# Kernel tuning notes

Hardware: AMD Instinct MI355X
Metric: run time of the kernel (lower is better)

## Reference

```python
import math
import jax, jax.numpy as jnp
import numpy as np

B, N, D, O = 8, 2048, 128, 128


def setup_inputs() -> dict:
    key = jax.random.key(0)
    ks = jax.random.split(key, 8)
    s = 1.0 / math.sqrt(D)
    x = jax.random.normal(ks[0], (B, N, D), dtype=jnp.float32)
    A = jax.random.bernoulli(ks[1], 0.02, (B, N, N)).astype(jnp.float32)
    W_qk = jax.random.normal(ks[2], (D, D), dtype=jnp.float32) * s
    b_qk = jnp.zeros((D,), dtype=jnp.float32)
    W_l = jax.random.normal(ks[3], (D, O), dtype=jnp.float32) * s
    b_l = jnp.zeros((O,), dtype=jnp.float32)
    W_r = jax.random.normal(ks[4], (D, O), dtype=jnp.float32) * s
    W_d = jax.random.normal(ks[5], (1, D), dtype=jnp.float32)
    b_d = jnp.zeros((D,), dtype=jnp.float32)
    return {"x": x, "A": A, "W_qk": W_qk, "b_qk": b_qk, "W_l": W_l,
            "b_l": b_l, "W_r": W_r, "W_d": W_d, "b_d": b_d}


def reference(x, A, W_qk, b_qk, W_l, b_l, W_r, W_d, b_d):
    d = x.shape[-1]
    # degree gate: sigmoid(Linear(deg)) scales features
    deg = jnp.sum(A, axis=-1, keepdims=True)              # (B,N,1)
    gate = jax.nn.sigmoid(deg @ W_d + b_d)                # (B,N,D)
    xg = x * gate                                         # (B,N,D)
    # sigmoid QK projection and dense NxN scores
    QK = jax.nn.sigmoid(xg @ W_qk + b_qk)                 # (B,N,D)
    scores = jnp.einsum('bnd,bmd->bnm', QK, QK) / jnp.sqrt(jnp.float32(d))
    scores = scores * A                                   # adjacency mask
    attn = scores / (jnp.sum(scores, axis=-1, keepdims=True) + 1e-6)
    agg = jnp.einsum('bnm,bmd->bnd', attn, xg)            # (B,N,D)
    out = agg @ W_l + b_l + xg @ W_r                      # (B,N,O)
    # F.normalize(p=2, dim=-1): x / max(||x||, eps)
    nrm = jnp.linalg.norm(out, axis=-1, keepdims=True)
    return out / jnp.maximum(nrm, 1e-12)
```

## Files before the change

### kernel.cpp

```cpp
#include <hip/hip_runtime.h>
#include <hip/hip_bf16.h>

#define B_ 8
#define N_ 2048
#define D_ 128
#define NROW (B_*N_)

typedef __bf16 bf16;
typedef __bf16 bf16x8 __attribute__((ext_vector_type(8)));
typedef float f32x4 __attribute__((ext_vector_type(4)));
typedef float f32x16 __attribute__((ext_vector_type(16)));

__device__ __forceinline__ float sigmoidf_(float x) {
    return 1.0f / (1.0f + __expf(-x));
}

__device__ __forceinline__ void g2l16(const bf16* g, void* l) {
    __builtin_amdgcn_global_load_lds(
        (const __attribute__((address_space(1))) unsigned int*)g,
        (__attribute__((address_space(3))) unsigned int*)l, 16, 0, 0);
}

__device__ __forceinline__ unsigned pk_bf16(float a, float b) {
    union { bf16 h[2]; unsigned u; } t;
    t.h[0] = (bf16)a; t.h[1] = (bf16)b;
    return t.u;
}

__global__ __launch_bounds__(256) void k_wtrans(const float* __restrict__ Wqk,
        const float* __restrict__ Wl, const float* __restrict__ Wr,
        bf16* __restrict__ wqkT, bf16* __restrict__ wlT, bf16* __restrict__ wrT) {
    int m = blockIdx.x >> 3;
    int chunk = blockIdx.x & 7;
    const float* W = (m == 0) ? Wqk : (m == 1 ? Wl : Wr);
    bf16* WT = (m == 0) ? wqkT : (m == 1 ? wlT : wrT);
#pragma unroll
    for (int e = 0; e < 8; ++e) {
        int idx = e * 256 + threadIdx.x;
        int ol = idx >> 7;
        int i  = idx & 127;
        int o = chunk * 16 + ol;
        WT[o * 128 + i] = (bf16)W[i * 128 + o];
    }
}

__global__ __launch_bounds__(256) void k_deg_mask(const float* __restrict__ A,
        unsigned int* __restrict__ mask, float* __restrict__ deg) {
    const int row = blockIdx.x;
    const float* a = A + (size_t)row * N_;
    const int t = threadIdx.x, w = t >> 6, lane = t & 63;
    __shared__ int partial[4];
    int cnt = 0;
    unsigned int* mrow = mask + (size_t)row * (N_ / 32);
#pragma unroll
    for (int i = 0; i < N_ / 1024; ++i) {
        float4 v = *(const float4*)(a + i * 1024 + t * 4);
        unsigned long long nib = (unsigned long long)((v.x != 0.f) | ((v.y != 0.f) << 1) |
                                                      ((v.z != 0.f) << 2) | ((v.w != 0.f) << 3));
        unsigned long long p = nib << ((t & 15) * 4);
        p |= __shfl_xor(p, 1);
        p |= __shfl_xor(p, 2);
        p |= __shfl_xor(p, 4);
        p |= __shfl_xor(p, 8);
        if ((t & 15) == 0) {
            int idx = i * 32 + (t >> 4) * 2;
            mrow[idx] = (unsigned int)p;
            mrow[idx + 1] = (unsigned int)(p >> 32);
            cnt += __popcll(p);
        }
    }
    cnt += __shfl_xor(cnt, 16);
    cnt += __shfl_xor(cnt, 32);
    if (lane == 0) partial[w] = cnt;
    __syncthreads();
    if (t == 0) deg[row] = (float)(partial[0] + partial[1] + partial[2] + partial[3]);
}

__global__ __launch_bounds__(256) void k_proj(const float* __restrict__ x,
        const float* __restrict__ deg, const float* __restrict__ Wd,
        const float* __restrict__ bd, const bf16* __restrict__ wqkT,
        const float* __restrict__ bqk,
        bf16* __restrict__ qkG, bf16* __restrict__ xgG, bf16* __restrict__ xgTG) {
    __shared__ bf16 wq[128][136];
    __shared__ bf16 xgl[64][136];
    const int t = threadIdx.x, lane = t & 63, w = t >> 6;
    const int rowbase = blockIdx.x * 64;
    {
        int r = t >> 1, h = t & 1;
        const bf16* src = wqkT + r * 128 + h * 64;
#pragma unroll
        for (int k = 0; k < 64; k += 8)
            *(bf16x8*)&wq[r][h * 64 + k] = *(const bf16x8*)(src + k);
    }
#pragma unroll
    for (int e = 0; e < 32; ++e) {
        int idx = e * 256 + t;
        int rl = idx >> 7;
        int d  = idx & 127;
        size_t fr = (size_t)rowbase + rl;
        float g = sigmoidf_(deg[fr] * Wd[d] + bd[d]);
        float v = x[fr * 128 + d] * g;
        bf16 bv = (bf16)v;
        xgl[rl][d] = bv;
        xgG[fr * 128 + d] = bv;
    }
    __syncthreads();
    const int cIdx = lane & 15, g4 = lane >> 4;
    bf16x8 ax[4];
#pragma unroll
    for (int c = 0; c < 4; ++c)
        ax[c] = *(const bf16x8*)&xgl[w * 16 + cIdx][c * 32 + g4 * 8];
#pragma unroll
    for (int dsub = 0; dsub < 8; ++dsub) {
        f32x4 acc = {0.f, 0.f, 0.f, 0.f};
#pragma unroll
        for (int c = 0; c < 4; ++c) {
            bf16x8 bw = *(const bf16x8*)&wq[dsub * 16 + cIdx][c * 32 + g4 * 8];
            acc = __builtin_amdgcn_mfma_f32_16x16x32_bf16(ax[c], bw, acc, 0, 0, 0);
        }
        int col = dsub * 16 + cIdx;
        float bb = bqk[col];
#pragma unroll
        for (int r = 0; r < 4; ++r) {
            size_t row = (size_t)rowbase + w * 16 + g4 * 4 + r;
            qkG[row * 128 + col] = (bf16)sigmoidf_(acc[r] + bb);
        }
    }
    {
        int b = rowbase / N_;
        int nbase = rowbase % N_;
#pragma unroll
        for (int e = 0; e < 32; ++e) {
            int idx = e * 256 + t;
            int d  = idx >> 6;
            int nl = idx & 63;
            xgTG[((size_t)b * 128 + d) * N_ + nbase + nl] = xgl[nl][d];
        }
    }
}

__global__ __launch_bounds__(512, 2) void k_attn(const bf16* __restrict__ qkG,
        const bf16* __restrict__ xgTG, const unsigned int* __restrict__ mask32,
        bf16* __restrict__ aggG) {
    __shared__ __align__(16) char LDSC[132096];
    const int t = threadIdx.x, l = t & 63, w = t >> 6;
    const int h = l >> 5, l31 = l & 31;
    const int q = w >> 1, s = w & 1;
    const int bid = (blockIdx.x & 7) * 32 + (blockIdx.x >> 3);
    const int b = bid >> 5;
    const int rowbase = (bid & 31) * 64;
    const int R0 = rowbase + s * 32;
    const float inv = 0.08838834764831845f;

    auto do_stage = [&](int jb, int bbuf) {
        char* qdst = LDSC + bbuf * 32768 + w * 4096;
        char* xdst = LDSC + 65536 + bbuf * 32768 + w * 4096;
#pragma unroll
        for (int i = 0; i < 4; ++i) {
            int G = w * 256 + i * 64 + l;
            int j = G >> 4, g = G & 15;
            const bf16* src = qkG + ((size_t)(b * N_ + jb + j)) * 128 + ((g ^ (j & 7)) << 3);
            g2l16(src, qdst + i * 1024);
            const bf16* src2 = xgTG + ((size_t)b * 128 + j) * N_ + jb + ((g ^ (j & 7)) << 3);
            g2l16(src2, xdst + i * 1024);
        }
    };

    bf16x8 qki[8];
    {
        const bf16* srcB = qkG + ((size_t)(b * N_ + R0 + l31)) * 128 + h * 8;
#pragma unroll
        for (int sl = 0; sl < 8; ++sl) qki[sl] = *(const bf16x8*)(srcB + sl * 16);
    }
    const unsigned int* mrow = mask32 + ((size_t)(b * N_ + R0 + l31)) * (N_ / 32) + q;
    unsigned int mw = mrow[0];

    do_stage(0, 0);
    __syncthreads();

    f32x16 num[4]; num[0] = f32x16{}; num[1] = f32x16{}; num[2] = f32x16{}; num[3] = f32x16{};
    float rs = 0.f;

    for (int ts = 0; ts < 16; ++ts) {
        const int bb = ts & 1;
        unsigned int mw_n = 0;
        if (ts < 15) {
            mw_n = mrow[(ts + 1) * 4];
            do_stage((ts + 1) * 128, bb ^ 1);
        }
        const char* qb = LDSC + bb * 32768;
        const char* xb = LDSC + 65536 + bb * 32768;
        f32x16 st{};
        const int rowb = (q * 32 + l31) * 256;
#pragma unroll
        for (int sl = 0; sl < 8; ++sl) {
            bf16x8 aj = *(const bf16x8*)(qb + rowb + ((((sl << 1) | h) ^ (l & 7)) << 4));
            st = __builtin_amdgcn_mfma_f32_32x32x16_bf16(aj, qki[sl], st, 0, 0, 0);
        }
        unsigned int mws = mw >> (h * 4);
        unsigned int wpk[8];
#pragma unroll
        for (int r2 = 0; r2 < 8; ++r2) {
            const int r = r2 * 2;
            const int bit0 = (r & 3) + 8 * (r >> 2);
            float p0 = ((mws >> bit0) & 1u) ? st[r] * inv : 0.f;
            float p1 = ((mws >> (bit0 + 1)) & 1u) ? st[r + 1] * inv : 0.f;
            rs += p0 + p1;
            wpk[r2] = pk_bf16(p0, p1);
        }
        union { unsigned int u[4]; bf16x8 v; } pa0, pa1;
        pa0.u[0] = wpk[0]; pa0.u[1] = wpk[1]; pa0.u[2] = wpk[2]; pa0.u[3] = wpk[3];
        pa1.u[0] = wpk[4]; pa1.u[1] = wpk[5]; pa1.u[2] = wpk[6]; pa1.u[3] = wpk[7];
        const int xr = l & 7;
#pragma unroll
        for (int c = 0; c < 4; ++c) {
            const char* rowp = xb + (c * 32 + l31) * 256;
            union { unsigned long long d2[2]; bf16x8 v; } b0, b1;
            b0.d2[0] = *(const unsigned long long*)(rowp + (((q * 4 + 0) ^ xr) << 4) + (h << 3));
            b0.d2[1] = *(const unsigned long long*)(rowp + (((q * 4 + 1) ^ xr) << 4) + (h << 3));
            b1.d2[0] = *(const unsigned long long*)(rowp + (((q * 4 + 2) ^ xr) << 4) + (h << 3));
            b1.d2[1] = *(const unsigned long long*)(rowp + (((q * 4 + 3) ^ xr) << 4) + (h << 3));
            num[c] = __builtin_amdgcn_mfma_f32_32x32x16_bf16(pa0.v, b0.v, num[c], 0, 0, 0);
            num[c] = __builtin_amdgcn_mfma_f32_32x32x16_bf16(pa1.v, b1.v, num[c], 0, 0, 0);
        }
        mw = mw_n;
        __syncthreads();
    }

    rs += __shfl_xor(rs, 32);
    float* RSB = (float*)(LDSC + 131072);
    if (l < 32) RSB[(s * 32 + l31) * 4 + q] = rs;
    float* PART = (float*)LDSC;
#pragma unroll
    for (int c = 0; c < 4; ++c)
#pragma unroll
        for (int r = 0; r < 16; ++r) {
            int m = (r & 3) + 8 * (r >> 2) + 4 * h;
            PART[q * 8192 + (s * 32 + m) * 128 + c * 32 + l31] = num[c][r];
        }
    __syncthreads();
    {
        int row = t >> 3, colbase = (t & 7) * 16;
        float accv[16];
#pragma unroll
        for (int k = 0; k < 16; ++k) accv[k] = 0.f;
#pragma unroll
        for (int q4 = 0; q4 < 4; ++q4)
#pragma unroll
            for (int k = 0; k < 4; ++k) {
                f32x4 pv = *(const f32x4*)(PART + q4 * 8192 + row * 128 + colbase + k * 4);
                accv[k * 4 + 0] += pv[0]; accv[k * 4 + 1] += pv[1];
                accv[k * 4 + 2] += pv[2]; accv[k * 4 + 3] += pv[3];
            }
        float den = RSB[row * 4 + 0] + RSB[row * 4 + 1] + RSB[row * 4 + 2] + RSB[row * 4 + 3] + 1e-6f;
        float sc = 1.0f / den;
        bf16x8 o0, o1;
#pragma unroll
        for (int k = 0; k < 8; ++k) { o0[k] = (bf16)(accv[k] * sc); o1[k] = (bf16)(accv[8 + k] * sc); }
        bf16* dst = aggG + ((size_t)(b * N_ + rowbase + row)) * 128 + colbase;
        *(bf16x8*)dst = o0;
        *(bf16x8*)(dst + 8) = o1;
    }
}

__global__ __launch_bounds__(256) void k_out(const bf16* __restrict__ aggG,
        const bf16* __restrict__ xgG, const bf16* __restrict__ wlT,
        const bf16* __restrict__ wrT, const float* __restrict__ blv,
        float* __restrict__ out) {
    __shared__ bf16 wl[128][136];
    __shared__ bf16 wr[128][136];
    __shared__ bf16 ag[64][136];
    __shared__ bf16 xgl[64][136];
    const int t = threadIdx.x, lane = t & 63, w = t >> 6;
    const int rowbase = blockIdx.x * 64;
    {
        int r = t >> 1, h = t & 1;
#pragma unroll
        for (int k = 0; k < 64; k += 8) {
            *(bf16x8*)&wl[r][h * 64 + k] = *(const bf16x8*)(wlT + r * 128 + h * 64 + k);
            *(bf16x8*)&wr[r][h * 64 + k] = *(const bf16x8*)(wrT + r * 128 + h * 64 + k);
        }
        int rl = t >> 2, q = t & 3;
        const bf16* s1 = aggG + ((size_t)(rowbase + rl)) * 128 + q * 32;
        const bf16* s2 = xgG + ((size_t)(rowbase + rl)) * 128 + q * 32;
#pragma unroll
        for (int k = 0; k < 32; k += 8) {
            *(bf16x8*)&ag[rl][q * 32 + k] = *(const bf16x8*)(s1 + k);
            *(bf16x8*)&xgl[rl][q * 32 + k] = *(const bf16x8*)(s2 + k);
        }
    }
    __syncthreads();
    const int cIdx = lane & 15, g4 = lane >> 4;
    bf16x8 aa[4], ax[4];
#pragma unroll
    for (int c = 0; c < 4; ++c) {
        aa[c] = *(const bf16x8*)&ag[w * 16 + cIdx][c * 32 + g4 * 8];
        ax[c] = *(const bf16x8*)&xgl[w * 16 + cIdx][c * 32 + g4 * 8];
    }
    f32x4 acc[8];
    float ss[4] = {0.f, 0.f, 0.f, 0.f};
#pragma unroll
    for (int osub = 0; osub < 8; ++osub) {
        float bb = blv[osub * 16 + cIdx];
        f32x4 a = {bb, bb, bb, bb};
#pragma unroll
        for (int c = 0; c < 4; ++c) {
            bf16x8 b1 = *(const bf16x8*)&wl[osub * 16 + cIdx][c * 32 + g4 * 8];
            a = __builtin_amdgcn_mfma_f32_16x16x32_bf16(aa[c], b1, a, 0, 0, 0);
            bf16x8 b2 = *(const bf16x8*)&wr[osub * 16 + cIdx][c * 32 + g4 * 8];
            a = __builtin_amdgcn_mfma_f32_16x16x32_bf16(ax[c], b2, a, 0, 0, 0);
        }
        acc[osub] = a;
#pragma unroll
        for (int r = 0; r < 4; ++r) ss[r] += a[r] * a[r];
    }
#pragma unroll
    for (int r = 0; r < 4; ++r) {
        ss[r] += __shfl_xor(ss[r], 1);
        ss[r] += __shfl_xor(ss[r], 2);
        ss[r] += __shfl_xor(ss[r], 4);
        ss[r] += __shfl_xor(ss[r], 8);
    }
    float sc[4];
#pragma unroll
    for (int r = 0; r < 4; ++r) sc[r] = 1.0f / fmaxf(sqrtf(ss[r]), 1e-12f);
#pragma unroll
    for (int osub = 0; osub < 8; ++osub)
#pragma unroll
        for (int r = 0; r < 4; ++r) {
            size_t row = (size_t)rowbase + w * 16 + g4 * 4 + r;
            out[row * 128 + osub * 16 + cIdx] = acc[osub][r] * sc[r];
        }
}

extern "C" void kernel_launch(void* const* d_in, const int* in_sizes, int n_in,
                              void* d_out, int out_size, void* d_ws, size_t ws_size,
                              hipStream_t stream) {
    const float* x   = (const float*)d_in[0];
    const float* A   = (const float*)d_in[1];
    const float* Wqk = (const float*)d_in[2];
    const float* bqk = (const float*)d_in[3];
    const float* Wl  = (const float*)d_in[4];
    const float* bl  = (const float*)d_in[5];
    const float* Wr  = (const float*)d_in[6];
    const float* Wd  = (const float*)d_in[7];
    const float* bd  = (const float*)d_in[8];
    float* out = (float*)d_out;
    char* ws = (char*)d_ws;

    unsigned int* maskG = (unsigned int*)ws;
    float* degG = (float*)(ws + (4 << 20));
    bf16* wqkT  = (bf16*)(ws + (5 << 20));
    bf16* wlT   = (bf16*)(ws + (5 << 20) + 32768);
    bf16* wrT   = (bf16*)(ws + (5 << 20) + 65536);
    bf16* qkG   = (bf16*)(ws + (6 << 20));
    bf16* xgG   = (bf16*)(ws + (10 << 20));
    bf16* xgTG  = (bf16*)(ws + (14 << 20));
    bf16* aggG  = (bf16*)(ws + (18 << 20));

    hipLaunchKernelGGL(k_wtrans, dim3(24), dim3(256), 0, stream, Wqk, Wl, Wr, wqkT, wlT, wrT);
    hipLaunchKernelGGL(k_deg_mask, dim3(NROW), dim3(256), 0, stream, A, maskG, degG);
    hipLaunchKernelGGL(k_proj, dim3(NROW / 64), dim3(256), 0, stream,
                       x, degG, Wd, bd, wqkT, bqk, qkG, xgG, xgTG);
    hipLaunchKernelGGL(k_attn, dim3(NROW / 64), dim3(512), 0, stream, qkG, xgTG, maskG, aggG);
    hipLaunchKernelGGL(k_out, dim3(NROW / 64), dim3(256), 0, stream, aggG, xgG, wlT, wrT, bl, out);
}
```

Baseline: 255.2 us.

## Fuse output projection into attention kernel and make degree/mask one row per wave

The output projection and L2 normalization are folded into the attention kernel: the normalized aggregate is kept in LDS instead of being written to global memory and reloaded by a separate kernel. The eight waves split the 64x128 output tile by row and column halves and combine their partial squared norms through LDS. Separately, the degree/mask kernel now handles one adjacency row per wave, which removes the shared-memory reduction and the block barrier. This saves a kernel launch and the aggregate's global round trip, but enlarges LDS usage in the attention kernel, which may reduce occupancy.

```diff
diff --git a/kernel.cpp b/kernel.cpp
--- a/kernel.cpp
+++ b/kernel.cpp
@@ -46,24 +46,23 @@
 
 __global__ __launch_bounds__(256) void k_deg_mask(const float* __restrict__ A,
         unsigned int* __restrict__ mask, float* __restrict__ deg) {
-    const int row = blockIdx.x;
+    const int w = threadIdx.x >> 6, lane = threadIdx.x & 63;
+    const int row = blockIdx.x * 4 + w;
     const float* a = A + (size_t)row * N_;
-    const int t = threadIdx.x, w = t >> 6, lane = t & 63;
-    __shared__ int partial[4];
+    unsigned int* mrow = mask + (size_t)row * (N_ / 32);
     int cnt = 0;
-    unsigned int* mrow = mask + (size_t)row * (N_ / 32);
-#pragma unroll
-    for (int i = 0; i < N_ / 1024; ++i) {
-        float4 v = *(const float4*)(a + i * 1024 + t * 4);
+#pragma unroll
+    for (int i = 0; i < N_ / 256; ++i) {
+        float4 v = *(const float4*)(a + i * 256 + lane * 4);
         unsigned long long nib = (unsigned long long)((v.x != 0.f) | ((v.y != 0.f) << 1) |
                                                       ((v.z != 0.f) << 2) | ((v.w != 0.f) << 3));
-        unsigned long long p = nib << ((t & 15) * 4);
+        unsigned long long p = nib << ((lane & 15) * 4);
         p |= __shfl_xor(p, 1);
         p |= __shfl_xor(p, 2);
         p |= __shfl_xor(p, 4);
         p |= __shfl_xor(p, 8);
-        if ((t & 15) == 0) {
-            int idx = i * 32 + (t >> 4) * 2;
+        if ((lane & 15) == 0) {
+            int idx = i * 8 + (lane >> 4) * 2;
             mrow[idx] = (unsigned int)p;
             mrow[idx + 1] = (unsigned int)(p >> 32);
             cnt += __popcll(p);
@@ -71,9 +70,7 @@
     }
     cnt += __shfl_xor(cnt, 16);
     cnt += __shfl_xor(cnt, 32);
-    if (lane == 0) partial[w] = cnt;
-    __syncthreads();
-    if (t == 0) deg[row] = (float)(partial[0] + partial[1] + partial[2] + partial[3]);
+    if (lane == 0) deg[row] = (float)cnt;
 }
 
 __global__ __launch_bounds__(256) void k_proj(const float* __restrict__ x,
@@ -139,10 +136,12 @@
     }
 }
 
-__global__ __launch_bounds__(512, 2) void k_attn(const bf16* __restrict__ qkG,
+__global__ __launch_bounds__(512, 2) void k_attn_out(const bf16* __restrict__ qkG,
         const bf16* __restrict__ xgTG, const unsigned int* __restrict__ mask32,
-        bf16* __restrict__ aggG) {
-    __shared__ __align__(16) char LDSC[132096];
+        const bf16* __restrict__ xgG, const bf16* __restrict__ wlT,
+        const bf16* __restrict__ wrT, const float* __restrict__ blv,
+        float* __restrict__ out) {
+    __shared__ __align__(16) char LDSC[149504];
     const int t = threadIdx.x, l = t & 63, w = t >> 6;
     const int h = l >> 5, l31 = l & 31;
     const int q = w >> 1, s = w & 1;
@@ -257,80 +256,85 @@
         bf16x8 o0, o1;
 #pragma unroll
         for (int k = 0; k < 8; ++k) { o0[k] = (bf16)(accv[k] * sc); o1[k] = (bf16)(accv[8 + k] * sc); }
-        bf16* dst = aggG + ((size_t)(b * N_ + rowbase + row)) * 128 + colbase;
-        *(bf16x8*)dst = o0;
-        *(bf16x8*)(dst + 8) = o1;
-    }
-}
-
-__global__ __launch_bounds__(256) void k_out(const bf16* __restrict__ aggG,
-        const bf16* __restrict__ xgG, const bf16* __restrict__ wlT,
-        const bf16* __restrict__ wrT, const float* __restrict__ blv,
-        float* __restrict__ out) {
-    __shared__ bf16 wl[128][136];
-    __shared__ bf16 wr[128][136];
-    __shared__ bf16 ag[64][136];
-    __shared__ bf16 xgl[64][136];
-    const int t = threadIdx.x, lane = t & 63, w = t >> 6;
-    const int rowbase = blockIdx.x * 64;
-    {
-        int r = t >> 1, h = t & 1;
-#pragma unroll
-        for (int k = 0; k < 64; k += 8) {
-            *(bf16x8*)&wl[r][h * 64 + k] = *(const bf16x8*)(wlT + r * 128 + h * 64 + k);
-            *(bf16x8*)&wr[r][h * 64 + k] = *(const bf16x8*)(wrT + r * 128 + h * 64 + k);
-        }
-        int rl = t >> 2, q = t & 3;
-        const bf16* s1 = aggG + ((size_t)(rowbase + rl)) * 128 + q * 32;
-        const bf16* s2 = xgG + ((size_t)(rowbase + rl)) * 128 + q * 32;
+        char* AGL = LDSC + 132096;
+        *(bf16x8*)(AGL + row * 272 + colbase * 2) = o0;
+        *(bf16x8*)(AGL + row * 272 + colbase * 2 + 16) = o1;
+    }
+    __syncthreads();
+    {
+        bf16* wlds = (bf16*)LDSC;
+        bf16* wrds = (bf16*)(LDSC + 34816);
+        bf16* xgl  = (bf16*)(LDSC + 69632);
+        int r = t >> 2, hq = t & 3;
+        const bf16* s1 = wlT + r * 128 + hq * 32;
+        const bf16* s2 = wrT + r * 128 + hq * 32;
 #pragma unroll
         for (int k = 0; k < 32; k += 8) {
-            *(bf16x8*)&ag[rl][q * 32 + k] = *(const bf16x8*)(s1 + k);
-            *(bf16x8*)&xgl[rl][q * 32 + k] = *(const bf16x8*)(s2 + k);
-        }
-    }
-    __syncthreads();
-    const int cIdx = lane & 15, g4 = lane >> 4;
-    bf16x8 aa[4], ax[4];
-#pragma unroll
-    for (int c = 0; c < 4; ++c) {
-        aa[c] = *(const bf16x8*)&ag[w * 16 + cIdx][c * 32 + g4 * 8];
-        ax[c] = *(const bf16x8*)&xgl[w * 16 + cIdx][c * 32 + g4 * 8];
-    }
-    f32x4 acc[8];
-    float ss[4] = {0.f, 0.f, 0.f, 0.f};
-#pragma unroll
-    for (int osub = 0; osub < 8; ++osub) {
-        float bb = blv[osub * 16 + cIdx];
-        f32x4 a = {bb, bb, bb, bb};
+            *(bf16x8*)&wlds[r * 136 + hq * 32 + k] = *(const bf16x8*)(s1 + k);
+            *(bf16x8*)&wrds[r * 136 + hq * 32 + k] = *(const bf16x8*)(s2 + k);
+        }
+        int rl = t >> 3, cb = (t & 7) * 16;
+        const bf16* s3 = xgG + ((size_t)(b * N_ + rowbase + rl)) * 128 + cb;
+        *(bf16x8*)&xgl[rl * 136 + cb] = *(const bf16x8*)s3;
+        *(bf16x8*)&xgl[rl * 136 + cb + 8] = *(const bf16x8*)(s3 + 8);
+    }
+    __syncthreads();
+    {
+        const bf16* wlds = (const bf16*)LDSC;
+        const bf16* wrds = (const bf16*)(LDSC + 34816);
+        const bf16* xgl  = (const bf16*)(LDSC + 69632);
+        const bf16* AGLb = (const bf16*)(LDSC + 132096);
+        float* SSB = (float*)(LDSC + 87040);
+        const int cIdx = l & 15, g4 = l >> 4;
+        const int rt = (w & 3) * 16;
+        const int oh = w >> 2;
+        bf16x8 aa[4], ax[4];
 #pragma unroll
         for (int c = 0; c < 4; ++c) {
-            bf16x8 b1 = *(const bf16x8*)&wl[osub * 16 + cIdx][c * 32 + g4 * 8];
-            a = __builtin_amdgcn_mfma_f32_16x16x32_bf16(aa[c], b1, a, 0, 0, 0);
-            bf16x8 b2 = *(const bf16x8*)&wr[osub * 16 + cIdx][c * 32 + g4 * 8];
-            a = __builtin_amdgcn_mfma_f32_16x16x32_bf16(ax[c], b2, a, 0, 0, 0);
-        }
-        acc[osub] = a;
-#pragma unroll
-        for (int r = 0; r < 4; ++r) ss[r] += a[r] * a[r];
-    }
-#pragma unroll
-    for (int r = 0; r < 4; ++r) {
-        ss[r] += __shfl_xor(ss[r], 1);
-        ss[r] += __shfl_xor(ss[r], 2);
-        ss[r] += __shfl_xor(ss[r], 4);
-        ss[r] += __shfl_xor(ss[r], 8);
-    }
-    float sc[4];
-#pragma unroll
-    for (int r = 0; r < 4; ++r) sc[r] = 1.0f / fmaxf(sqrtf(ss[r]), 1e-12f);
-#pragma unroll
-    for (int osub = 0; osub < 8; ++osub)
+            aa[c] = *(const bf16x8*)(AGLb + (rt + cIdx) * 136 + c * 32 + g4 * 8);
+            ax[c] = *(const bf16x8*)(xgl + (rt + cIdx) * 136 + c * 32 + g4 * 8);
+        }
+        f32x4 acc[4];
+        float ss[4] = {0.f, 0.f, 0.f, 0.f};
+#pragma unroll
+        for (int os = 0; os < 4; ++os) {
+            int col = (oh * 4 + os) * 16 + cIdx;
+            float bb = blv[col];
+            f32x4 a = {bb, bb, bb, bb};
+#pragma unroll
+            for (int c = 0; c < 4; ++c) {
+                bf16x8 b1 = *(const bf16x8*)(wlds + col * 136 + c * 32 + g4 * 8);
+                a = __builtin_amdgcn_mfma_f32_16x16x32_bf16(aa[c], b1, a, 0, 0, 0);
+                bf16x8 b2 = *(const bf16x8*)(wrds + col * 136 + c * 32 + g4 * 8);
+                a = __builtin_amdgcn_mfma_f32_16x16x32_bf16(ax[c], b2, a, 0, 0, 0);
+            }
+            acc[os] = a;
+#pragma unroll
+            for (int r = 0; r < 4; ++r) ss[r] += a[r] * a[r];
+        }
 #pragma unroll
         for (int r = 0; r < 4; ++r) {
-            size_t row = (size_t)rowbase + w * 16 + g4 * 4 + r;
-            out[row * 128 + osub * 16 + cIdx] = acc[osub][r] * sc[r];
-        }
+            ss[r] += __shfl_xor(ss[r], 1);
+            ss[r] += __shfl_xor(ss[r], 2);
+            ss[r] += __shfl_xor(ss[r], 4);
+            ss[r] += __shfl_xor(ss[r], 8);
+        }
+        if (cIdx == 0)
+#pragma unroll
+            for (int r = 0; r < 4; ++r) SSB[oh * 64 + rt + g4 * 4 + r] = ss[r];
+        __syncthreads();
+#pragma unroll
+        for (int r = 0; r < 4; ++r) {
+            int row_l = rt + g4 * 4 + r;
+            float tot = SSB[row_l] + SSB[64 + row_l];
+            float sc = 1.0f / fmaxf(sqrtf(tot), 1e-12f);
+#pragma unroll
+            for (int os = 0; os < 4; ++os) {
+                size_t grow = (size_t)(b * N_ + rowbase + row_l);
+                out[grow * 128 + (oh * 4 + os) * 16 + cIdx] = acc[os][r] * sc;
+            }
+        }
+    }
 }
 
 extern "C" void kernel_launch(void* const* d_in, const int* in_sizes, int n_in,
@@ -356,12 +360,11 @@
     bf16* qkG   = (bf16*)(ws + (6 << 20));
     bf16* xgG   = (bf16*)(ws + (10 << 20));
     bf16* xgTG  = (bf16*)(ws + (14 << 20));
-    bf16* aggG  = (bf16*)(ws + (18 << 20));
 
     hipLaunchKernelGGL(k_wtrans, dim3(24), dim3(256), 0, stream, Wqk, Wl, Wr, wqkT, wlT, wrT);
-    hipLaunchKernelGGL(k_deg_mask, dim3(NROW), dim3(256), 0, stream, A, maskG, degG);
+    hipLaunchKernelGGL(k_deg_mask, dim3(NROW / 4), dim3(256), 0, stream, A, maskG, degG);
     hipLaunchKernelGGL(k_proj, dim3(NROW / 64), dim3(256), 0, stream,
                        x, degG, Wd, bd, wqkT, bqk, qkG, xgG, xgTG);
-    hipLaunchKernelGGL(k_attn, dim3(NROW / 64), dim3(512), 0, stream, qkG, xgTG, maskG, aggG);
-    hipLaunchKernelGGL(k_out, dim3(NROW / 64), dim3(256), 0, stream, aggG, xgG, wlT, wrT, bl, out);
-}
+    hipLaunchKernelGGL(k_attn_out, dim3(NROW / 64), dim3(512), 0, stream,
+                       qkG, xgTG, maskG, xgG, wlT, wrT, bl, out);
+}
```

New measurement: 253.9 us. About the same (-0.5%).
